# Kernel tuning notes

Measured on AMD Instinct MI355X. Metric: run time of the kernel, lower is better.

## Reference

```python
import jax, jax.numpy as jnp
import numpy as np

B, T, IN = 32, 1024, 256
H = 128          # hidden_size
NL = 2           # num_layers
NC = 4           # num_classes
F2 = 2 * H       # bidirectional feature size


def _lstm_dir(xs, w_ih, w_hh, b_ih, b_hh, reverse):
    # xs: [T, B, in]; w_ih: [4H, in]; w_hh: [4H, H]
    if reverse:
        xs = xs[::-1]
    h0 = jnp.zeros((xs.shape[1], H), xs.dtype)
    c0 = jnp.zeros((xs.shape[1], H), xs.dtype)

    def step(carry, xt):
        h, c = carry
        g = xt @ w_ih.T + b_ih + h @ w_hh.T + b_hh  # [B, 4H]
        i, f, gg, o = jnp.split(g, 4, axis=-1)       # PyTorch gate order i,f,g,o
        c = jax.nn.sigmoid(f) * c + jax.nn.sigmoid(i) * jnp.tanh(gg)
        h = jax.nn.sigmoid(o) * jnp.tanh(c)
        return (h, c), h

    _, hs = jax.lax.scan(step, (h0, c0), xs)  # [T, B, H]
    if reverse:
        hs = hs[::-1]
    return hs


def setup_inputs() -> dict:
    key = jax.random.key(0)
    ks = jax.random.split(key, 12)
    s = 0.05
    x = jax.random.normal(ks[0], (B, T, IN), jnp.float32)
    # stacked LSTM params: [layer, direction, ...]; layer0 in = IN, layer1 in = 2H = IN
    w_ih = jax.random.normal(ks[1], (NL, 2, 4 * H, IN), jnp.float32) * s
    w_hh = jax.random.normal(ks[2], (NL, 2, 4 * H, H), jnp.float32) * s
    b_ih = jax.random.normal(ks[3], (NL, 2, 4 * H), jnp.float32) * s
    b_hh = jax.random.normal(ks[4], (NL, 2, 4 * H), jnp.float32) * s
    wq = jax.random.normal(ks[5], (F2, F2), jnp.float32) * s
    wk = jax.random.normal(ks[6], (F2, F2), jnp.float32) * s
    wv = jax.random.normal(ks[7], (F2, F2), jnp.float32) * s
    bq = jax.random.normal(ks[8], (F2,), jnp.float32) * s
    bk = jax.random.normal(ks[9], (F2,), jnp.float32) * s
    bv = jax.random.normal(ks[10], (F2,), jnp.float32) * s
    w_fc = jax.random.normal(ks[11], (NC, F2), jnp.float32) * s
    b_fc = jnp.zeros((NC,), jnp.float32)
    return {"x": x, "w_ih": w_ih, "w_hh": w_hh, "b_ih": b_ih, "b_hh": b_hh,
            "wq": wq, "wk": wk, "wv": wv, "bq": bq, "bk": bk, "bv": bv,
            "w_fc": w_fc, "b_fc": b_fc}


def reference(x, w_ih, w_hh, b_ih, b_hh, wq, wk, wv, bq, bk, bv, w_fc, b_fc):
    # --- biLSTM (eval mode: inter-layer dropout inactive) ---
    xs = jnp.swapaxes(x, 0, 1)  # time-major [T, B, IN]
    for l in range(NL):
        fwd = _lstm_dir(xs, w_ih[l, 0], w_hh[l, 0], b_ih[l, 0], b_hh[l, 0], False)
        bwd = _lstm_dir(xs, w_ih[l, 1], w_hh[l, 1], b_ih[l, 1], b_hh[l, 1], True)
        xs = jnp.concatenate([fwd, bwd], axis=-1)  # [T, B, 2H]
    out = jnp.swapaxes(xs, 0, 1)  # [B, T, 2H]
    # --- naive full self-attention ---
    q = out @ wq.T + bq
    k = out @ wk.T + bk
    v = out @ wv.T + bv
    scores = jnp.einsum('btd,bsd->bts', q, k) / jnp.sqrt(jnp.float32(F2))
    attn = jax.nn.softmax(scores, axis=-1)          # [B, T, T]
    ctx = jnp.einsum('bts,bsd->btd', attn, v)       # [B, T, 2H]
    # --- FC head on last timestep ---
    return ctx[:, -1, :] @ w_fc.T + b_fc            # [B, NC]
```

## Files before the change

kernel.cpp:

```cpp
#include <hip/hip_runtime.h>
#include <math.h>
#include <stdint.h>

#define BB 32
#define TT 1024
#define INF 256
#define HH 128
#define G4 512
#define CH 16

typedef _Float16 half2_t __attribute__((ext_vector_type(2)));
typedef __attribute__((address_space(3))) uint32_t lds_u32;
typedef __attribute__((address_space(1))) const uint32_t glb_u32;

__device__ __forceinline__ float fdot2f(half2_t a, half2_t b, float c) {
    return __builtin_amdgcn_fdot2(a, b, c, false);
}
__device__ __forceinline__ float rcpf(float x) {
    return __builtin_amdgcn_rcpf(x);
}
__device__ __forceinline__ float dpp_xor1(float x) {
    return __builtin_bit_cast(float, __builtin_amdgcn_update_dpp(
        0, __builtin_bit_cast(int, x), 0xB1, 0xF, 0xF, true));
}
__device__ __forceinline__ float dpp_xor2(float x) {
    return __builtin_bit_cast(float, __builtin_amdgcn_update_dpp(
        0, __builtin_bit_cast(int, x), 0x4E, 0xF, 0xF, true));
}
__device__ __forceinline__ void bar_lgkm() {
    asm volatile("s_waitcnt lgkmcnt(0)\n\ts_barrier" ::: "memory");
}

__global__ __launch_bounds__(256, 2) void gemm_inproj(
    const float* __restrict__ A,
    const float* __restrict__ w_ih_l,
    const float* __restrict__ b_ih_l,
    const float* __restrict__ b_hh_l,
    float* __restrict__ xproj)
{
    const int d  = blockIdx.z;
    const float* W = w_ih_l + (size_t)d * G4 * INF;
    float* C = xproj + (size_t)d * 32768 * 512;
    const int m0 = blockIdx.y * 128;
    const int n0 = blockIdx.x * 128;
    const int tid = threadIdx.x;
    const int tx = tid & 15, ty = tid >> 4;

    __shared__ __align__(16) half2_t As2[16 * 128];
    __shared__ __align__(16) half2_t Bs2[16 * 128];

    float acc[8][8] = {};
    const int lr = tid >> 1;
    const int lk = (tid & 1) * 16;

    float4 ar4[4], br4[4];
#pragma unroll
    for (int i = 0; i < 4; ++i) {
        ar4[i] = *(const float4*)(A + (size_t)(m0 + lr) * 256 + lk + 4 * i);
        br4[i] = *(const float4*)(W + (size_t)(n0 + lr) * 256 + lk + 4 * i);
    }

    for (int k0 = 0; k0 < 256; k0 += 32) {
        __syncthreads();
#pragma unroll
        for (int i = 0; i < 4; ++i) {
            const int kp = (lk >> 1) + 2 * i;
            As2[(kp + 0) * 128 + lr] = half2_t{(_Float16)ar4[i].x, (_Float16)ar4[i].y};
            As2[(kp + 1) * 128 + lr] = half2_t{(_Float16)ar4[i].z, (_Float16)ar4[i].w};
            Bs2[(kp + 0) * 128 + lr] = half2_t{(_Float16)br4[i].x, (_Float16)br4[i].y};
            Bs2[(kp + 1) * 128 + lr] = half2_t{(_Float16)br4[i].z, (_Float16)br4[i].w};
        }
        __syncthreads();
        if (k0 + 32 < 256) {
#pragma unroll
            for (int i = 0; i < 4; ++i) {
                ar4[i] = *(const float4*)(A + (size_t)(m0 + lr) * 256 + k0 + 32 + lk + 4 * i);
                br4[i] = *(const float4*)(W + (size_t)(n0 + lr) * 256 + k0 + 32 + lk + 4 * i);
            }
        }
#pragma unroll
        for (int kp = 0; kp < 16; ++kp) {
            half2_t av[8], bv[8];
            *(float4*)&av[0] = *(const float4*)&As2[kp * 128 + ty * 4];
            *(float4*)&av[4] = *(const float4*)&As2[kp * 128 + 64 + ty * 4];
            *(float4*)&bv[0] = *(const float4*)&Bs2[kp * 128 + tx * 4];
            *(float4*)&bv[4] = *(const float4*)&Bs2[kp * 128 + 64 + tx * 4];
#pragma unroll
            for (int i = 0; i < 8; ++i)
#pragma unroll
                for (int j = 0; j < 8; ++j)
                    acc[i][j] = fdot2f(av[i], bv[j], acc[i][j]);
        }
    }

    float bias[8];
#pragma unroll
    for (int j = 0; j < 8; ++j) {
        const int n = n0 + (j < 4 ? tx * 4 + j : 64 + tx * 4 + (j - 4));
        bias[j] = b_ih_l[d * G4 + n] + b_hh_l[d * G4 + n];
    }
#pragma unroll
    for (int i = 0; i < 8; ++i) {
        const int m = m0 + (i < 4 ? ty * 4 + i : 64 + ty * 4 + (i - 4));
        float4 o0, o1;
        o0.x = acc[i][0] + bias[0]; o0.y = acc[i][1] + bias[1];
        o0.z = acc[i][2] + bias[2]; o0.w = acc[i][3] + bias[3];
        o1.x = acc[i][4] + bias[4]; o1.y = acc[i][5] + bias[5];
        o1.z = acc[i][6] + bias[6]; o1.w = acc[i][7] + bias[7];
        *(float4*)(C + (size_t)m * 512 + n0 + tx * 4)      = o0;
        *(float4*)(C + (size_t)m * 512 + n0 + 64 + tx * 4) = o1;
    }
}

__global__ __launch_bounds__(512, 1) void lstm_rec(
    const float* __restrict__ xproj,
    const float* __restrict__ w_hh_l,
    float* __restrict__ out)
{
    const int b = blockIdx.x & 31;
    const int d = blockIdx.x >> 5;
    const int tid = threadIdx.x;
    const int wvid = tid >> 6;
    const int l = tid & 63;
    const int s = l & 3;
    const int g = l >> 2;
    const int j = (wvid << 4) | g;

    __shared__ __align__(16) _Float16 hs[HH];
    __shared__ __align__(16) float xbuf[2][CH * 512];
    __shared__ __align__(16) float obuf[CH * HH];

    half2_t wv[4][16];
#pragma unroll
    for (int G = 0; G < 4; ++G) {
        const float* wr = w_hh_l + (size_t)(d * G4 + 128 * G + j) * HH + 32 * s;
#pragma unroll
        for (int q4 = 0; q4 < 8; ++q4) {
            float4 f = *(const float4*)(wr + 4 * q4);
            wv[G][2 * q4]     = half2_t{(_Float16)f.x, (_Float16)f.y};
            wv[G][2 * q4 + 1] = half2_t{(_Float16)f.z, (_Float16)f.w};
        }
    }

    if (tid < 64) ((half2_t*)hs)[tid] = half2_t{(_Float16)0.f, (_Float16)0.f};
    float c = 0.f;

    const float* xp = xproj + ((size_t)d * BB + b) * TT * 512;
    float* ob = out + (size_t)b * TT * 256 + d * HH;

    {
        const int tlo = d ? 1008 : 0;
        const float* gsrc = xp + (size_t)tlo * 512;
#pragma unroll
        for (int i = 0; i < 4; ++i)
            __builtin_amdgcn_global_load_lds((glb_u32*)(gsrc + tid * 4 + i * 2048),
                                             (lds_u32*)&xbuf[0][tid * 4 + i * 2048],
                                             16, 0, 0);
    }
    __syncthreads();

    for (int ck = 0; ck < 64; ++ck) {
        const int cur = ck & 1;
        if (ck + 1 < 64) {
            const int tlo = d ? (1008 - (ck + 1) * CH) : (ck + 1) * CH;
            const float* gsrc = xp + (size_t)tlo * 512;
#pragma unroll
            for (int i = 0; i < 4; ++i)
                __builtin_amdgcn_global_load_lds((glb_u32*)(gsrc + tid * 4 + i * 2048),
                                                 (lds_u32*)&xbuf[cur ^ 1][tid * 4 + i * 2048],
                                                 16, 0, 0);
        }
        const float* xb = xbuf[cur];

#pragma unroll 1
        for (int si = 0; si < CH; ++si) {
            const int lds_t = d ? (CH - 1 - si) : si;

            const float xi = xb[lds_t * 512 +       j];
            const float xf = xb[lds_t * 512 + 128 + j];
            const float xg = xb[lds_t * 512 + 256 + j];
            const float xo = xb[lds_t * 512 + 384 + j];

            const float4* hp = (const float4*)(hs + 32 * s);
            float4 hA = hp[0], hB = hp[1], hC = hp[2], hD = hp[3];
            half2_t hh[16];
            hh[0]  = __builtin_bit_cast(half2_t, hA.x);
            hh[1]  = __builtin_bit_cast(half2_t, hA.y);
            hh[2]  = __builtin_bit_cast(half2_t, hA.z);
            hh[3]  = __builtin_bit_cast(half2_t, hA.w);
            hh[4]  = __builtin_bit_cast(half2_t, hB.x);
            hh[5]  = __builtin_bit_cast(half2_t, hB.y);
            hh[6]  = __builtin_bit_cast(half2_t, hB.z);
            hh[7]  = __builtin_bit_cast(half2_t, hB.w);
            hh[8]  = __builtin_bit_cast(half2_t, hC.x);
            hh[9]  = __builtin_bit_cast(half2_t, hC.y);
            hh[10] = __builtin_bit_cast(half2_t, hC.z);
            hh[11] = __builtin_bit_cast(half2_t, hC.w);
            hh[12] = __builtin_bit_cast(half2_t, hD.x);
            hh[13] = __builtin_bit_cast(half2_t, hD.y);
            hh[14] = __builtin_bit_cast(half2_t, hD.z);
            hh[15] = __builtin_bit_cast(half2_t, hD.w);

            float a0 = 0.f, a1 = 0.f, a2 = 0.f, a3 = 0.f;
            float e0 = 0.f, e1 = 0.f, e2 = 0.f, e3 = 0.f;
#pragma unroll
            for (int kk = 0; kk < 8; ++kk) {
                a0 = fdot2f(wv[0][kk], hh[kk], a0);
                a1 = fdot2f(wv[1][kk], hh[kk], a1);
                a2 = fdot2f(wv[2][kk], hh[kk], a2);
                a3 = fdot2f(wv[3][kk], hh[kk], a3);
                e0 = fdot2f(wv[0][kk + 8], hh[kk + 8], e0);
                e1 = fdot2f(wv[1][kk + 8], hh[kk + 8], e1);
                e2 = fdot2f(wv[2][kk + 8], hh[kk + 8], e2);
                e3 = fdot2f(wv[3][kk + 8], hh[kk + 8], e3);
            }
            a0 += e0; a1 += e1; a2 += e2; a3 += e3;

            a0 += dpp_xor1(a0); a0 += dpp_xor2(a0);
            a1 += dpp_xor1(a1); a1 += dpp_xor2(a1);
            a2 += dpp_xor1(a2); a2 += dpp_xor2(a2);
            a3 += dpp_xor1(a3); a3 += dpp_xor2(a3);

            const float gi = rcpf(1.f + __expf(-(a0 + xi)));
            const float gf = rcpf(1.f + __expf(-(a1 + xf)));
            const float gg = 1.f - 2.f * rcpf(1.f + __expf(2.f * (a2 + xg)));
            const float go = rcpf(1.f + __expf(-(a3 + xo)));
            c = gf * c + gi * gg;
            const float th = 1.f - 2.f * rcpf(1.f + __expf(2.f * c));
            const float h = go * th;
            if (s == 0) {
                hs[j] = (_Float16)h;
                obuf[si * HH + j] = h;
            }
            bar_lgkm();
        }

        {
            const int idx = tid * 4;
            const int sf = idx >> 7, jf = idx & 127;
            const int sg = ck * CH + sf;
            const int t  = d ? (TT - 1 - sg) : sg;
            float4 o0 = *(const float4*)&obuf[idx];
            *(float4*)&ob[(size_t)t * 256 + jf] = o0;
        }
        __syncthreads();
    }
}

__global__ __launch_bounds__(256) void attn_kernel(
    const float* __restrict__ out1,
    const float* __restrict__ wq, const float* __restrict__ bq,
    const float* __restrict__ wk,
    const float* __restrict__ wv, const float* __restrict__ bv,
    const float* __restrict__ wfc, const float* __restrict__ bfc,
    float* __restrict__ outp)
{
    const int b = blockIdx.x;
    const int tid = threadIdx.x;
    __shared__ float xl[256], q[256], u[256], cx[256];
    __shared__ __align__(16) float r[256];
    __shared__ float sc[TT];
    __shared__ float red[256];

    const float* ob = out1 + (size_t)b * TT * 256;

    xl[tid] = ob[(size_t)(TT - 1) * 256 + tid];
    __syncthreads();

    float acc = bq[tid];
    const float* wqr = wq + (size_t)tid * 256;
#pragma unroll 4
    for (int k = 0; k < 256; ++k) acc += xl[k] * wqr[k];
    q[tid] = acc;
    __syncthreads();

    acc = 0.f;
#pragma unroll 4
    for (int dd = 0; dd < 256; ++dd) acc += q[dd] * wk[(size_t)dd * 256 + tid];
    r[tid] = acc;
    __syncthreads();

    const int wave = tid >> 6, lane = tid & 63;
    float4 r4 = *(const float4*)&r[lane * 4];
    for (int t = wave; t < TT; t += 4) {
        float4 o4 = *(const float4*)(ob + (size_t)t * 256 + lane * 4);
        float p = r4.x * o4.x + r4.y * o4.y + r4.z * o4.z + r4.w * o4.w;
#pragma unroll
        for (int off = 32; off > 0; off >>= 1) p += __shfl_down(p, off, 64);
        if (lane == 0) sc[t] = p * 0.0625f;
    }
    __syncthreads();

    float mx = -1e30f;
#pragma unroll
    for (int i = 0; i < 4; ++i) mx = fmaxf(mx, sc[tid + 256 * i]);
    red[tid] = mx; __syncthreads();
    for (int st = 128; st > 0; st >>= 1) {
        if (tid < st) red[tid] = fmaxf(red[tid], red[tid + st]);
        __syncthreads();
    }
    mx = red[0]; __syncthreads();
    float lsum = 0.f;
#pragma unroll
    for (int i = 0; i < 4; ++i) {
        float e = expf(sc[tid + 256 * i] - mx);
        sc[tid + 256 * i] = e;
        lsum += e;
    }
    __syncthreads();
    red[tid] = lsum; __syncthreads();
    for (int st = 128; st > 0; st >>= 1) {
        if (tid < st) red[tid] += red[tid + st];
        __syncthreads();
    }
    const float inv = 1.f / red[0];
    __syncthreads();

    acc = 0.f;
#pragma unroll 8
    for (int t = 0; t < TT; ++t) acc += sc[t] * ob[(size_t)t * 256 + tid];
    u[tid] = acc * inv;
    __syncthreads();

    acc = bv[tid];
#pragma unroll 4
    for (int k = 0; k < 256; ++k) acc += u[k] * wv[(size_t)tid * 256 + k];
    cx[tid] = acc;
    __syncthreads();

    if (tid < 4) {
        float o = bfc[tid];
        for (int k = 0; k < 256; ++k) o += cx[k] * wfc[tid * 256 + k];
        outp[b * 4 + tid] = o;
    }
}

extern "C" void kernel_launch(void* const* d_in, const int* in_sizes, int n_in,
                              void* d_out, int out_size, void* d_ws, size_t ws_size,
                              hipStream_t stream)
{
    const float* x    = (const float*)d_in[0];
    const float* w_ih = (const float*)d_in[1];
    const float* w_hh = (const float*)d_in[2];
    const float* b_ih = (const float*)d_in[3];
    const float* b_hh = (const float*)d_in[4];
    const float* wq   = (const float*)d_in[5];
    const float* wk   = (const float*)d_in[6];
    const float* wv   = (const float*)d_in[7];
    const float* bq   = (const float*)d_in[8];
    const float* bv   = (const float*)d_in[10];
    const float* wfc  = (const float*)d_in[11];
    const float* bfcv = (const float*)d_in[12];
    float* outp = (float*)d_out;

    float* ws    = (float*)d_ws;
    float* xproj = ws;
    float* out0  = ws + 33554432;
    float* out1  = out0 + 8388608;

    dim3 gg(4, 256, 2);

    gemm_inproj<<<gg, 256, 0, stream>>>(x, w_ih, b_ih, b_hh, xproj);
    lstm_rec<<<64, 512, 0, stream>>>(xproj, w_hh, out0);
    gemm_inproj<<<gg, 256, 0, stream>>>(out0, w_ih + 2 * 512 * 256, b_ih + 1024, b_hh + 1024, xproj);
    lstm_rec<<<64, 512, 0, stream>>>(xproj, w_hh + 2 * 512 * 128, out1);
    attn_kernel<<<32, 256, 0, stream>>>(out1, wq, bq, wk, wv, bv, wfc, bfcv, outp);
}
```

Measured before the change: 1.783 ms.

## Batch LSTM recurrence over 16 sequences per block using MFMA

```diff
diff --git a/kernel.cpp b/kernel.cpp
--- a/kernel.cpp
+++ b/kernel.cpp
@@ -7,25 +7,16 @@
 #define INF 256
 #define HH 128
 #define G4 512
-#define CH 16
 
 typedef _Float16 half2_t __attribute__((ext_vector_type(2)));
-typedef __attribute__((address_space(3))) uint32_t lds_u32;
-typedef __attribute__((address_space(1))) const uint32_t glb_u32;
+typedef _Float16 f16x8 __attribute__((ext_vector_type(8)));
+typedef float f32x4 __attribute__((ext_vector_type(4)));
 
 __device__ __forceinline__ float fdot2f(half2_t a, half2_t b, float c) {
     return __builtin_amdgcn_fdot2(a, b, c, false);
 }
 __device__ __forceinline__ float rcpf(float x) {
     return __builtin_amdgcn_rcpf(x);
-}
-__device__ __forceinline__ float dpp_xor1(float x) {
-    return __builtin_bit_cast(float, __builtin_amdgcn_update_dpp(
-        0, __builtin_bit_cast(int, x), 0xB1, 0xF, 0xF, true));
-}
-__device__ __forceinline__ float dpp_xor2(float x) {
-    return __builtin_bit_cast(float, __builtin_amdgcn_update_dpp(
-        0, __builtin_bit_cast(int, x), 0x4E, 0xF, 0xF, true));
 }
 __device__ __forceinline__ void bar_lgkm() {
     asm volatile("s_waitcnt lgkmcnt(0)\n\ts_barrier" ::: "memory");
@@ -40,7 +31,7 @@
 {
     const int d  = blockIdx.z;
     const float* W = w_ih_l + (size_t)d * G4 * INF;
-    float* C = xproj + (size_t)d * 32768 * 512;
+    float* C = xproj + (size_t)d * 1024 * 512 * 32;
     const int m0 = blockIdx.y * 128;
     const int n0 = blockIdx.x * 128;
     const int tid = threadIdx.x;
@@ -53,11 +44,14 @@
     const int lr = tid >> 1;
     const int lk = (tid & 1) * 16;
 
+    const int mrow = m0 + lr;
+    const size_t arow = ((size_t)(mrow & 31) * 1024 + (size_t)(mrow >> 5)) * INF;
+
     float4 ar4[4], br4[4];
 #pragma unroll
     for (int i = 0; i < 4; ++i) {
-        ar4[i] = *(const float4*)(A + (size_t)(m0 + lr) * 256 + lk + 4 * i);
-        br4[i] = *(const float4*)(W + (size_t)(n0 + lr) * 256 + lk + 4 * i);
+        ar4[i] = *(const float4*)(A + arow + lk + 4 * i);
+        br4[i] = *(const float4*)(W + (size_t)(n0 + lr) * INF + lk + 4 * i);
     }
 
     for (int k0 = 0; k0 < 256; k0 += 32) {
@@ -74,8 +68,8 @@
         if (k0 + 32 < 256) {
 #pragma unroll
             for (int i = 0; i < 4; ++i) {
-                ar4[i] = *(const float4*)(A + (size_t)(m0 + lr) * 256 + k0 + 32 + lk + 4 * i);
-                br4[i] = *(const float4*)(W + (size_t)(n0 + lr) * 256 + k0 + 32 + lk + 4 * i);
+                ar4[i] = *(const float4*)(A + arow + k0 + 32 + lk + 4 * i);
+                br4[i] = *(const float4*)(W + (size_t)(n0 + lr) * INF + k0 + 32 + lk + 4 * i);
             }
         }
 #pragma unroll
@@ -100,15 +94,20 @@
         bias[j] = b_ih_l[d * G4 + n] + b_hh_l[d * G4 + n];
     }
 #pragma unroll
-    for (int i = 0; i < 8; ++i) {
-        const int m = m0 + (i < 4 ? ty * 4 + i : 64 + ty * 4 + (i - 4));
-        float4 o0, o1;
-        o0.x = acc[i][0] + bias[0]; o0.y = acc[i][1] + bias[1];
-        o0.z = acc[i][2] + bias[2]; o0.w = acc[i][3] + bias[3];
-        o1.x = acc[i][4] + bias[4]; o1.y = acc[i][5] + bias[5];
-        o1.z = acc[i][6] + bias[6]; o1.w = acc[i][7] + bias[7];
-        *(float4*)(C + (size_t)m * 512 + n0 + tx * 4)      = o0;
-        *(float4*)(C + (size_t)m * 512 + n0 + 64 + tx * 4) = o1;
+    for (int q = 0; q < 2; ++q) {
+        const int rbase = q * 64 + ty * 4;
+        const int t = (m0 >> 5) + (rbase >> 5);
+        const int b = rbase & 31;
+#pragma unroll
+        for (int j = 0; j < 8; ++j) {
+            const int n = n0 + (j < 4 ? tx * 4 + j : 64 + tx * 4 + (j - 4));
+            float4 v;
+            v.x = acc[q * 4 + 0][j] + bias[j];
+            v.y = acc[q * 4 + 1][j] + bias[j];
+            v.z = acc[q * 4 + 2][j] + bias[j];
+            v.w = acc[q * 4 + 3][j] + bias[j];
+            *(float4*)(C + ((size_t)t * 512 + n) * 32 + b) = v;
+        }
     }
 }
 
@@ -117,133 +116,91 @@
     const float* __restrict__ w_hh_l,
     float* __restrict__ out)
 {
-    const int b = blockIdx.x & 31;
-    const int d = blockIdx.x >> 5;
+    const int d  = blockIdx.x >> 1;
+    const int hb = blockIdx.x & 1;
     const int tid = threadIdx.x;
-    const int wvid = tid >> 6;
+    const int w = tid >> 6;
     const int l = tid & 63;
-    const int s = l & 3;
-    const int g = l >> 2;
-    const int j = (wvid << 4) | g;
-
-    __shared__ __align__(16) _Float16 hs[HH];
-    __shared__ __align__(16) float xbuf[2][CH * 512];
-    __shared__ __align__(16) float obuf[CH * HH];
-
-    half2_t wv[4][16];
-#pragma unroll
-    for (int G = 0; G < 4; ++G) {
-        const float* wr = w_hh_l + (size_t)(d * G4 + 128 * G + j) * HH + 32 * s;
-#pragma unroll
-        for (int q4 = 0; q4 < 8; ++q4) {
-            float4 f = *(const float4*)(wr + 4 * q4);
-            wv[G][2 * q4]     = half2_t{(_Float16)f.x, (_Float16)f.y};
-            wv[G][2 * q4 + 1] = half2_t{(_Float16)f.z, (_Float16)f.w};
-        }
-    }
-
-    if (tid < 64) ((half2_t*)hs)[tid] = half2_t{(_Float16)0.f, (_Float16)0.f};
-    float c = 0.f;
-
-    const float* xp = xproj + ((size_t)d * BB + b) * TT * 512;
-    float* ob = out + (size_t)b * TT * 256 + d * HH;
-
-    {
-        const int tlo = d ? 1008 : 0;
-        const float* gsrc = xp + (size_t)tlo * 512;
-#pragma unroll
-        for (int i = 0; i < 4; ++i)
-            __builtin_amdgcn_global_load_lds((glb_u32*)(gsrc + tid * 4 + i * 2048),
-                                             (lds_u32*)&xbuf[0][tid * 4 + i * 2048],
-                                             16, 0, 0);
-    }
-    __syncthreads();
-
-    for (int ck = 0; ck < 64; ++ck) {
-        const int cur = ck & 1;
-        if (ck + 1 < 64) {
-            const int tlo = d ? (1008 - (ck + 1) * CH) : (ck + 1) * CH;
-            const float* gsrc = xp + (size_t)tlo * 512;
-#pragma unroll
-            for (int i = 0; i < 4; ++i)
-                __builtin_amdgcn_global_load_lds((glb_u32*)(gsrc + tid * 4 + i * 2048),
-                                                 (lds_u32*)&xbuf[cur ^ 1][tid * 4 + i * 2048],
-                                                 16, 0, 0);
-        }
-        const float* xb = xbuf[cur];
-
-#pragma unroll 1
-        for (int si = 0; si < CH; ++si) {
-            const int lds_t = d ? (CH - 1 - si) : si;
-
-            const float xi = xb[lds_t * 512 +       j];
-            const float xf = xb[lds_t * 512 + 128 + j];
-            const float xg = xb[lds_t * 512 + 256 + j];
-            const float xo = xb[lds_t * 512 + 384 + j];
-
-            const float4* hp = (const float4*)(hs + 32 * s);
-            float4 hA = hp[0], hB = hp[1], hC = hp[2], hD = hp[3];
-            half2_t hh[16];
-            hh[0]  = __builtin_bit_cast(half2_t, hA.x);
-            hh[1]  = __builtin_bit_cast(half2_t, hA.y);
-            hh[2]  = __builtin_bit_cast(half2_t, hA.z);
-            hh[3]  = __builtin_bit_cast(half2_t, hA.w);
-            hh[4]  = __builtin_bit_cast(half2_t, hB.x);
-            hh[5]  = __builtin_bit_cast(half2_t, hB.y);
-            hh[6]  = __builtin_bit_cast(half2_t, hB.z);
-            hh[7]  = __builtin_bit_cast(half2_t, hB.w);
-            hh[8]  = __builtin_bit_cast(half2_t, hC.x);
-            hh[9]  = __builtin_bit_cast(half2_t, hC.y);
-            hh[10] = __builtin_bit_cast(half2_t, hC.z);
-            hh[11] = __builtin_bit_cast(half2_t, hC.w);
-            hh[12] = __builtin_bit_cast(half2_t, hD.x);
-            hh[13] = __builtin_bit_cast(half2_t, hD.y);
-            hh[14] = __builtin_bit_cast(half2_t, hD.z);
-            hh[15] = __builtin_bit_cast(half2_t, hD.w);
-
-            float a0 = 0.f, a1 = 0.f, a2 = 0.f, a3 = 0.f;
-            float e0 = 0.f, e1 = 0.f, e2 = 0.f, e3 = 0.f;
-#pragma unroll
-            for (int kk = 0; kk < 8; ++kk) {
-                a0 = fdot2f(wv[0][kk], hh[kk], a0);
-                a1 = fdot2f(wv[1][kk], hh[kk], a1);
-                a2 = fdot2f(wv[2][kk], hh[kk], a2);
-                a3 = fdot2f(wv[3][kk], hh[kk], a3);
-                e0 = fdot2f(wv[0][kk + 8], hh[kk + 8], e0);
-                e1 = fdot2f(wv[1][kk + 8], hh[kk + 8], e1);
-                e2 = fdot2f(wv[2][kk + 8], hh[kk + 8], e2);
-                e3 = fdot2f(wv[3][kk + 8], hh[kk + 8], e3);
-            }
-            a0 += e0; a1 += e1; a2 += e2; a3 += e3;
-
-            a0 += dpp_xor1(a0); a0 += dpp_xor2(a0);
-            a1 += dpp_xor1(a1); a1 += dpp_xor2(a1);
-            a2 += dpp_xor1(a2); a2 += dpp_xor2(a2);
-            a3 += dpp_xor1(a3); a3 += dpp_xor2(a3);
-
-            const float gi = rcpf(1.f + __expf(-(a0 + xi)));
-            const float gf = rcpf(1.f + __expf(-(a1 + xf)));
-            const float gg = 1.f - 2.f * rcpf(1.f + __expf(2.f * (a2 + xg)));
-            const float go = rcpf(1.f + __expf(-(a3 + xo)));
-            c = gf * c + gi * gg;
-            const float th = 1.f - 2.f * rcpf(1.f + __expf(2.f * c));
+    const int col = l & 15;
+    const int qg = l >> 4;
+    const int j = w * 16 + col;
+
+    __shared__ __align__(16) _Float16 hs2[2][16][136];
+
+    f16x8 wf[4][4];
+#pragma unroll
+    for (int G = 0; G < 4; ++G)
+#pragma unroll
+        for (int kc = 0; kc < 4; ++kc) {
+            const float* p = w_hh_l + (size_t)(d * G4 + G * HH + j) * HH + kc * 32 + qg * 8;
+            float4 f0 = *(const float4*)p;
+            float4 f1 = *(const float4*)(p + 4);
+            wf[G][kc] = f16x8{(_Float16)f0.x, (_Float16)f0.y, (_Float16)f0.z, (_Float16)f0.w,
+                              (_Float16)f1.x, (_Float16)f1.y, (_Float16)f1.z, (_Float16)f1.w};
+        }
+
+    for (int i = tid; i < 2 * 16 * 136; i += 512) ((_Float16*)hs2)[i] = (_Float16)0.f;
+    __syncthreads();
+
+    f32x4 c = {0.f, 0.f, 0.f, 0.f};
+    const float* xp = xproj + (size_t)d * 1024 * 512 * 32;
+    const int dt = d ? -1 : 1;
+    const int t0 = d ? (TT - 1) : 0;
+    const int xoff = hb * 16 + qg * 4;
+
+    float4 xc[4];
+#pragma unroll
+    for (int G = 0; G < 4; ++G)
+        xc[G] = *(const float4*)(xp + ((size_t)t0 * 512 + G * HH + j) * 32 + xoff);
+
+    for (int step = 0; step < TT; ++step) {
+        const int t = t0 + dt * step;
+        const int cur = step & 1, nxt = cur ^ 1;
+
+        bar_lgkm();
+
+        f16x8 af[4];
+#pragma unroll
+        for (int kc = 0; kc < 4; ++kc)
+            af[kc] = *(const f16x8*)&hs2[cur][col][kc * 32 + qg * 8];
+
+        float4 xn[4];
+        if (step + 1 < TT) {
+            const int tn = t + dt;
+#pragma unroll
+            for (int G = 0; G < 4; ++G)
+                xn[G] = *(const float4*)(xp + ((size_t)tn * 512 + G * HH + j) * 32 + xoff);
+        }
+
+        f32x4 ac[4];
+#pragma unroll
+        for (int G = 0; G < 4; ++G) {
+            f32x4 a = {0.f, 0.f, 0.f, 0.f};
+#pragma unroll
+            for (int kc = 0; kc < 4; ++kc)
+                a = __builtin_amdgcn_mfma_f32_16x16x32_f16(af[kc], wf[G][kc], a, 0, 0, 0);
+            ac[G] = a;
+        }
+
+        const float* x0 = (const float*)&xc[0];
+        const float* x1 = (const float*)&xc[1];
+        const float* x2 = (const float*)&xc[2];
+        const float* x3 = (const float*)&xc[3];
+#pragma unroll
+        for (int r = 0; r < 4; ++r) {
+            const float gi = rcpf(1.f + __expf(-(ac[0][r] + x0[r])));
+            const float gf = rcpf(1.f + __expf(-(ac[1][r] + x1[r])));
+            const float gg = 1.f - 2.f * rcpf(1.f + __expf(2.f * (ac[2][r] + x2[r])));
+            const float go = rcpf(1.f + __expf(-(ac[3][r] + x3[r])));
+            c[r] = gf * c[r] + gi * gg;
+            const float th = 1.f - 2.f * rcpf(1.f + __expf(2.f * c[r]));
             const float h = go * th;
-            if (s == 0) {
-                hs[j] = (_Float16)h;
-                obuf[si * HH + j] = h;
-            }
-            bar_lgkm();
-        }
-
-        {
-            const int idx = tid * 4;
-            const int sf = idx >> 7, jf = idx & 127;
-            const int sg = ck * CH + sf;
-            const int t  = d ? (TT - 1 - sg) : sg;
-            float4 o0 = *(const float4*)&obuf[idx];
-            *(float4*)&ob[(size_t)t * 256 + jf] = o0;
-        }
-        __syncthreads();
+            hs2[nxt][qg * 4 + r][j] = (_Float16)h;
+            const size_t bg = hb * 16 + qg * 4 + r;
+            out[bg * (size_t)(TT * 256) + (size_t)t * 256 + d * HH + j] = h;
+        }
+
+        xc[0] = xn[0]; xc[1] = xn[1]; xc[2] = xn[2]; xc[3] = xn[3];
     }
 }
 
@@ -361,8 +318,8 @@
     dim3 gg(4, 256, 2);
 
     gemm_inproj<<<gg, 256, 0, stream>>>(x, w_ih, b_ih, b_hh, xproj);
-    lstm_rec<<<64, 512, 0, stream>>>(xproj, w_hh, out0);
+    lstm_rec<<<4, 512, 0, stream>>>(xproj, w_hh, out0);
     gemm_inproj<<<gg, 256, 0, stream>>>(out0, w_ih + 2 * 512 * 256, b_ih + 1024, b_hh + 1024, xproj);
-    lstm_rec<<<64, 512, 0, stream>>>(xproj, w_hh + 2 * 512 * 128, out1);
+    lstm_rec<<<4, 512, 0, stream>>>(xproj, w_hh + 2 * 512 * 128, out1);
     attn_kernel<<<32, 256, 0, stream>>>(out1, wq, bq, wk, wv, bv, wfc, bfcv, outp);
 }
```

New measurement: 3.350 ms. 1.88x slower.
